# Performance work log

Measured on AMD Instinct MI355X. Metric: run time of the kernel, lower is better.

## Reference

```python
import jax, jax.numpy as jnp
import numpy as np

DIM, H, KVH = 1024, 16, 4
HD = DIM // H            # head_dim = 64
KV_DIM = KVH * HD        # 256
ROPE_BASE = 10000.0
EPS = 1e-6


def setup_inputs() -> dict:
    key = jax.random.key(0)
    ks = jax.random.split(key, 6)
    B, S = 4, 2048
    x = jax.random.normal(ks[0], (B, S, DIM), dtype=jnp.float32)
    sc = 0.02
    Wq = jax.random.normal(ks[1], (DIM, DIM), dtype=jnp.float32) * sc
    Wk = jax.random.normal(ks[2], (KV_DIM, DIM), dtype=jnp.float32) * sc
    Wv = jax.random.normal(ks[3], (KV_DIM, DIM), dtype=jnp.float32) * sc
    Wo = jax.random.normal(ks[4], (DIM, DIM), dtype=jnp.float32) * sc
    q_gain = jnp.full((H,), 1.5, dtype=jnp.float32)
    return {"x": x, "Wq": Wq, "Wk": Wk, "Wv": Wv, "Wo": Wo, "q_gain": q_gain}


def _rms_norm(t):
    return t * jax.lax.rsqrt(jnp.mean(t * t, axis=-1, keepdims=True) + EPS)


def _rotary(seqlen, dtype):
    inv_freq = 1.0 / (ROPE_BASE ** (jnp.arange(0, HD, 2, dtype=jnp.float32) / HD))
    t = jnp.arange(seqlen, dtype=jnp.float32)
    freqs = jnp.outer(t, inv_freq)                      # [S, HD/2]
    return jnp.cos(freqs).astype(dtype)[None, None], jnp.sin(freqs).astype(dtype)[None, None]


def _apply_rot(t, cos, sin):
    half = t.shape[-1] // 2
    t1, t2 = t[..., :half], t[..., half:]
    return jnp.concatenate((t1 * cos + t2 * sin, -t1 * sin + t2 * cos), axis=-1)


def reference(x, Wq, Wk, Wv, Wo, q_gain):
    B, S, D = x.shape
    q = (x @ Wq.T).reshape(B, S, H, HD).transpose(0, 2, 1, 3)      # [B,H,S,HD]
    k = (x @ Wk.T).reshape(B, S, KVH, HD).transpose(0, 2, 1, 3)    # [B,KVH,S,HD]
    v = (x @ Wv.T).reshape(B, S, KVH, HD).transpose(0, 2, 1, 3)
    q, k = _rms_norm(q), _rms_norm(k)
    cos, sin = _rotary(S, q.dtype)
    q, k = _apply_rot(q, cos, sin), _apply_rot(k, cos, sin)
    q = q * q_gain.astype(q.dtype)[None, :, None, None]
    rep = H // KVH
    k_exp = jnp.repeat(k, rep, axis=1)                              # GQA expand
    v_exp = jnp.repeat(v, rep, axis=1)
    scores = jnp.einsum('bhqd,bhkd->bhqk', q, k_exp) / np.sqrt(HD)
    causal = jnp.tril(jnp.ones((S, S), dtype=bool))
    scores = jnp.where(causal[None, None], scores, jnp.finfo(scores.dtype).min)
    attn = jax.nn.softmax(scores, axis=-1)
    y = jnp.einsum('bhqk,bhkd->bhqd', attn, v_exp)
    y = y.transpose(0, 2, 1, 3).reshape(B, S, D)
    return y @ Wo.T
```

## Files before the change

### kernel.cpp

```cpp
#include <hip/hip_runtime.h>

typedef float f32x4 __attribute__((ext_vector_type(4)));
typedef float f32x16 __attribute__((ext_vector_type(16)));
typedef __bf16 bf16x8 __attribute__((ext_vector_type(8)));
typedef unsigned short u16x8 __attribute__((ext_vector_type(8)));
typedef int i32x2 __attribute__((ext_vector_type(2)));
typedef int i32x4 __attribute__((ext_vector_type(4)));

#define DEV static __device__ __forceinline__

DEV float bf2f(unsigned short h) {
  unsigned int u = ((unsigned int)h) << 16;
  return __builtin_bit_cast(float, u);
}
DEV unsigned short f2bf(float f) {
  unsigned int u = __builtin_bit_cast(unsigned int, f);
  u += 0x7fff + ((u >> 16) & 1);
  return (unsigned short)(u >> 16);
}

DEV void g2l16(const void* g, void* l) {
  __builtin_amdgcn_global_load_lds(
      (const __attribute__((address_space(1))) void*)g,
      (__attribute__((address_space(3))) void*)l, 16, 0, 0);
}

DEV unsigned int cvtpk(float lo, float hi) {
  unsigned int r;
  asm("v_cvt_pk_bf16_f32 %0, %1, %2" : "=v"(r) : "v"(lo), "v"(hi));
  return r;
}

DEV float fexp2(float x) {
  float r;
  asm("v_exp_f32 %0, %1" : "=v"(r) : "v"(x));
  return r;
}

DEV void cvt8(const float* __restrict__ in, unsigned short* __restrict__ out, int idx) {
  int i = idx * 8;
  float4 a = *(const float4*)(in + i);
  float4 b = *(const float4*)(in + i + 4);
  u16x8 r;
  r[0] = f2bf(a.x); r[1] = f2bf(a.y); r[2] = f2bf(a.z); r[3] = f2bf(a.w);
  r[4] = f2bf(b.x); r[5] = f2bf(b.y); r[6] = f2bf(b.z); r[7] = f2bf(b.w);
  *(u16x8*)(out + i) = r;
}

__global__ __launch_bounds__(256) void k_cvt_all(const float* __restrict__ x,
                                                 const float* __restrict__ wq,
                                                 const float* __restrict__ wk,
                                                 const float* __restrict__ wv,
                                                 const float* __restrict__ wo,
                                                 unsigned short* __restrict__ xb,
                                                 unsigned short* __restrict__ wcat,
                                                 unsigned short* __restrict__ wob,
                                                 float2* __restrict__ rope) {
  const int blk = blockIdx.x, tid = threadIdx.x;
  if (blk < 4096) {
    cvt8(x, xb, blk * 256 + tid);
  } else if (blk < 4608) {
    cvt8(wq, wcat, (blk - 4096) * 256 + tid);
  } else if (blk < 4736) {
    cvt8(wk, wcat + 1048576, (blk - 4608) * 256 + tid);
  } else if (blk < 4864) {
    cvt8(wv, wcat + 1310720, (blk - 4736) * 256 + tid);
  } else if (blk < 5376) {
    cvt8(wo, wob, (blk - 4864) * 256 + tid);
  } else {
    int idx = (blk - 5376) * 256 + tid;
    int s = idx >> 5, dmod = idx & 31;
    float inv_freq = powf(10000.0f, -(float)dmod * (1.0f / 32.0f));
    float sn, cs;
    sincosf((float)s * inv_freq, &sn, &cs);
    rope[idx] = make_float2(cs, sn);
  }
}

__global__ __launch_bounds__(256) void k_qkv(const unsigned short* __restrict__ A,
                                             const unsigned short* __restrict__ B,
                                             const float* __restrict__ qg,
                                             const float2* __restrict__ rope,
                                             unsigned short* __restrict__ qn,
                                             unsigned short* __restrict__ kn2,
                                             unsigned short* __restrict__ vt2) {
  __shared__ unsigned short LDS[16384];
  unsigned short* As = LDS;
  unsigned short* Bs = LDS + 8192;
  const int K = 1024;
  const int tid = threadIdx.x;
  const int wid = tid >> 6, lane = tid & 63;
  const int g = lane >> 4, r16 = lane & 15;
  const int m0 = blockIdx.x * 128;
  const int y = blockIdx.y;
  const int n0 = y * 128;
  const int wr = wid >> 1, wc = wid & 1;

  f32x4 acc[4][4];
#pragma unroll
  for (int i = 0; i < 4; ++i)
#pragma unroll
    for (int j = 0; j < 4; ++j) acc[i][j] = f32x4{0.f, 0.f, 0.f, 0.f};

  const int cb = (lane & 7) * 16;

  for (int k0 = 0; k0 < K; k0 += 64) {
#pragma unroll
    for (int c = 0; c < 4; ++c) {
      int i = wid * 4 + c;
      int row = i * 8 + (lane >> 3);
      int sc = cb ^ ((row & 7) << 4);
      g2l16((const char*)A + ((size_t)(m0 + row) * K + k0) * 2 + sc, (char*)As + i * 1024);
      g2l16((const char*)B + ((size_t)(n0 + row) * K + k0) * 2 + sc, (char*)Bs + i * 1024);
    }
    __syncthreads();
#pragma unroll
    for (int kh = 0; kh < 2; ++kh) {
      bf16x8 af[4], bfr[4];
#pragma unroll
      for (int m = 0; m < 4; ++m) {
        int row = wr * 64 + m * 16 + r16;
        int byte = row * 128 + ((g * 16 + kh * 64) ^ ((row & 7) << 4));
        af[m] = *(const bf16x8*)((const char*)As + byte);
      }
#pragma unroll
      for (int n = 0; n < 4; ++n) {
        int row = wc * 64 + n * 16 + r16;
        int byte = row * 128 + ((g * 16 + kh * 64) ^ ((row & 7) << 4));
        bfr[n] = *(const bf16x8*)((const char*)Bs + byte);
      }
#pragma unroll
      for (int m = 0; m < 4; ++m)
#pragma unroll
        for (int n = 0; n < 4; ++n)
          acc[m][n] = __builtin_amdgcn_mfma_f32_16x16x32_bf16(af[m], bfr[n], acc[m][n], 0, 0, 0);
    }
    __syncthreads();
  }

  if (y < 10) {
    const bool isq = (y < 8);
    const int head = isq ? (2 * y + wc) : (2 * (y - 8) + wc);
    const float gain = isq ? qg[head] * 0.18033688011112042f : 1.0f;
    unsigned short* T = LDS;
#pragma unroll
    for (int m = 0; m < 4; ++m)
#pragma unroll
      for (int j = 0; j < 4; ++j) {
        int tokl = wr * 64 + m * 16 + g * 4 + j;
        int tok = m0 + tokl;
        int s = tok & 2047;
        float v0 = acc[m][0][j], v1 = acc[m][1][j], v2 = acc[m][2][j], v3 = acc[m][3][j];
        float ss = v0 * v0 + v1 * v1 + v2 * v2 + v3 * v3;
        ss += __shfl_xor(ss, 1); ss += __shfl_xor(ss, 2);
        ss += __shfl_xor(ss, 4); ss += __shfl_xor(ss, 8);
        float rs = rsqrtf(ss * (1.0f / 64.0f) + 1e-6f) * gain;
        float2 cs0 = rope[s * 32 + r16];
        float2 cs1 = rope[s * 32 + 16 + r16];
        float o0 = (v0 * cs0.x + v2 * cs0.y) * rs;
        float o2 = (v2 * cs0.x - v0 * cs0.y) * rs;
        float o1 = (v1 * cs1.x + v3 * cs1.y) * rs;
        float o3 = (v3 * cs1.x - v1 * cs1.y) * rs;
        char* rowb = (char*)T + tokl * 256;
        const int sw = (tokl & 15) << 4;
        const int dbase = wc * 128 + r16 * 2;
        *(unsigned short*)(rowb + ((dbase) ^ sw)) = f2bf(o0);
        *(unsigned short*)(rowb + ((dbase + 32) ^ sw)) = f2bf(o1);
        *(unsigned short*)(rowb + ((dbase + 64) ^ sw)) = f2bf(o2);
        *(unsigned short*)(rowb + ((dbase + 96) ^ sw)) = f2bf(o3);
      }
    __syncthreads();
    const int row0 = tid >> 4, cl = tid & 15;
    unsigned short* dstb = isq ? (qn + 2 * y * 64) : (kn2 + 2 * (y - 8) * 64);
    const int rstride = isq ? 1024 : 256;
#pragma unroll
    for (int it = 0; it < 8; ++it) {
      int row = it * 16 + row0;
      i32x4 w = *(const i32x4*)((const char*)T + row * 256 + ((cl * 16) ^ ((row & 15) << 4)));
      *(i32x4*)(dstb + (size_t)(m0 + row) * rstride + cl * 8) = w;
    }
  } else {
    unsigned short* T = LDS;
#pragma unroll
    for (int m = 0; m < 4; ++m)
#pragma unroll
      for (int n = 0; n < 4; ++n)
#pragma unroll
        for (int j = 0; j < 4; ++j) {
          int tokl = wr * 64 + m * 16 + g * 4 + j;
          int dl = wc * 64 + n * 16 + r16;
          int byte = (dl * 256 + tokl * 2) ^ ((dl & 15) << 4);
          *(unsigned short*)((char*)T + byte) = f2bf(acc[m][n][j]);
        }
    __syncthreads();
    const int d = tid >> 1, th = tid & 1;
    const int hv = 2 * (y - 10) + (d >> 6), dh = d & 63;
    const int bb = m0 >> 11;
    const int s0 = (m0 & 2047) + th * 64;
    const int kb64 = s0 >> 6;
    const int db = dh >> 5, d31 = dh & 31;
    const size_t vb0 = ((size_t)(bb * 4 + hv) * 32 + kb64) * 8 + db * 4;
    const int swz = (d & 15) << 4;
#pragma unroll
    for (int c = 0; c < 8; ++c) {
      i32x4 w = *(const i32x4*)((const char*)T + ((d * 256 + th * 128 + c * 16) ^ swz));
      *(i32x4*)(vt2 + (vb0 + (c >> 1)) * 512 + ((c & 1) * 32 + d31) * 8) = w;
    }
  }
}

__global__ __launch_bounds__(256) void k_krepack(const unsigned short* __restrict__ km,
                                                 unsigned short* __restrict__ kn2) {
  const int tid = threadIdx.x;
  const int bhv = blockIdx.y, kb = blockIdx.x;
  const int b = bhv >> 2, hv = bhv & 3;
  const int slot = tid & 63;
  const int m = tid >> 6;
  const int kw = slot & 31, hi8 = slot >> 5;
  const int key = kb * 32 + kw;
  const int d0 = m * 16 + hi8 * 8;
  u16x8 v = *(const u16x8*)(km + ((size_t)(b * 2048 + key)) * 256 + hv * 64 + d0);
  *(u16x8*)(kn2 + (((size_t)(bhv * 64 + kb) * 4 + m) * 512) + slot * 8) = v;
}

__global__ __launch_bounds__(256) void k_gemm_bt(const unsigned short* __restrict__ A,
                                                 const unsigned short* __restrict__ B,
                                                 float* __restrict__ C, int M, int N, int K) {
  __shared__ unsigned short As[128 * 64];
  __shared__ unsigned short Bs[128 * 64];
  const int tid = threadIdx.x;
  const int wid = tid >> 6, lane = tid & 63;
  const int g = lane >> 4, r16 = lane & 15;
  const int m0 = blockIdx.x * 128, n0 = blockIdx.y * 128;
  const int wr = wid >> 1, wc = wid & 1;

  f32x4 acc[4][4];
#pragma unroll
  for (int i = 0; i < 4; ++i)
#pragma unroll
    for (int j = 0; j < 4; ++j) acc[i][j] = f32x4{0.f, 0.f, 0.f, 0.f};

  const int cb = (lane & 7) * 16;

  for (int k0 = 0; k0 < K; k0 += 64) {
#pragma unroll
    for (int c = 0; c < 4; ++c) {
      int i = wid * 4 + c;
      int row = i * 8 + (lane >> 3);
      int sc = cb ^ ((row & 7) << 4);
      g2l16((const char*)A + ((size_t)(m0 + row) * K + k0) * 2 + sc, (char*)As + i * 1024);
      g2l16((const char*)B + ((size_t)(n0 + row) * K + k0) * 2 + sc, (char*)Bs + i * 1024);
    }
    __syncthreads();
#pragma unroll
    for (int kh = 0; kh < 2; ++kh) {
      bf16x8 af[4], bfr[4];
#pragma unroll
      for (int m = 0; m < 4; ++m) {
        int row = wr * 64 + m * 16 + r16;
        int byte = row * 128 + ((g * 16 + kh * 64) ^ ((row & 7) << 4));
        af[m] = *(const bf16x8*)((const char*)As + byte);
      }
#pragma unroll
      for (int n = 0; n < 4; ++n) {
        int row = wc * 64 + n * 16 + r16;
        int byte = row * 128 + ((g * 16 + kh * 64) ^ ((row & 7) << 4));
        bfr[n] = *(const bf16x8*)((const char*)Bs + byte);
      }
#pragma unroll
      for (int m = 0; m < 4; ++m)
#pragma unroll
        for (int n = 0; n < 4; ++n)
          acc[m][n] = __builtin_amdgcn_mfma_f32_16x16x32_bf16(af[m], bfr[n], acc[m][n], 0, 0, 0);
    }
    __syncthreads();
  }
#pragma unroll
  for (int m = 0; m < 4; ++m)
#pragma unroll
    for (int n = 0; n < 4; ++n)
#pragma unroll
      for (int j = 0; j < 4; ++j) {
        int row = m0 + wr * 64 + m * 16 + g * 4 + j;
        int col = n0 + wc * 64 + n * 16 + r16;
        C[(size_t)row * N + col] = acc[m][n][j];
      }
}

__global__ __launch_bounds__(512) void k_attn2(const unsigned short* __restrict__ qn,
                                               const unsigned short* __restrict__ kn2,
                                               const unsigned short* __restrict__ vt2,
                                               unsigned short* __restrict__ yb) {
  __shared__ unsigned short SMEM[4 * 8192];
  const int tid = threadIdx.x;
  const int wid = tid >> 6, lane = tid & 63;
  const int hi = lane >> 5, l31 = lane & 31;
  const int flat = blockIdx.x;
  const int qcx = 7 - (flat >> 6);
  const int bh = flat & 63;
  const int b = bh >> 4, h = bh & 15, hv = h >> 2;
  const int q0w = qcx * 256 + wid * 32;
  const int qglob = q0w + l31;
  const int tdiag = (q0w + 31) >> 6;
  const size_t tok0 = (size_t)b * 2048;

  const u16x8 onesu = {0x3F80, 0x3F80, 0x3F80, 0x3F80, 0x3F80, 0x3F80, 0x3F80, 0x3F80};
  const bf16x8 ones = __builtin_bit_cast(bf16x8, onesu);

  bf16x8 qf[4];
#pragma unroll
  for (int m = 0; m < 4; ++m)
    qf[m] = *(const bf16x8*)(qn + (tok0 + qglob) * 1024 + h * 64 + m * 16 + hi * 8);

  f32x16 oacc[2], lacc, zer;
#pragma unroll
  for (int r = 0; r < 16; ++r) { oacc[0][r] = 0.f; oacc[1][r] = 0.f; lacc[r] = 0.f; zer[r] = 0.f; }

  const int c0 = wid * 2;
  const unsigned short* src0;
  if (wid < 4) {
    src0 = kn2 + (size_t)(b * 4 + hv) * 131072 + c0 * 512 + lane * 8;
  } else {
    src0 = vt2 + (size_t)(b * 4 + hv) * 131072 + (c0 - 8) * 512 + lane * 8;
  }
  const unsigned short* src1 = src0 + 512;

  auto stage = [&](int T, int tb) {
    char* dst = (char*)SMEM + tb * 16384 + c0 * 1024;
    g2l16(src0 + (size_t)T * 4096, dst);
    g2l16(src1 + (size_t)T * 4096, dst + 1024);
  };

  const char* lbase = (const char*)SMEM + lane * 16;

  auto qk_tile = [&](int tb, f32x16* s) {
    const char* base = lbase + tb * 16384;
#pragma unroll
    for (int kt = 0; kt < 2; ++kt) {
      __builtin_amdgcn_s_setprio(1);
      bf16x8 kf = *(const bf16x8*)(base + (kt * 4) * 1024);
      f32x16 a = __builtin_amdgcn_mfma_f32_32x32x16_bf16(kf, qf[0], zer, 0, 0, 0);
#pragma unroll
      for (int m = 1; m < 4; ++m) {
        kf = *(const bf16x8*)(base + (kt * 4 + m) * 1024);
        a = __builtin_amdgcn_mfma_f32_32x32x16_bf16(kf, qf[m], a, 0, 0, 0);
      }
      __builtin_amdgcn_s_setprio(0);
      s[kt] = a;
    }
  };

  auto mask_tile = [&](int t, f32x16* s) {
    const int k0 = t * 64;
#pragma unroll
    for (int kt = 0; kt < 2; ++kt)
#pragma unroll
      for (int r = 0; r < 16; ++r) {
        int key = k0 + kt * 32 + (r & 3) + 8 * (r >> 2) + 4 * hi;
        if (key > qglob) s[kt][r] = -INFINITY;
      }
  };

  auto softmax_cvt = [&](f32x16* s, i32x4* paw) {
#pragma unroll
    for (int kt = 0; kt < 2; ++kt)
#pragma unroll
      for (int r = 0; r < 16; ++r) s[kt][r] = fexp2(s[kt][r]);
#pragma unroll
    for (int kt = 0; kt < 2; ++kt)
#pragma unroll
      for (int half = 0; half < 2; ++half) {
        int bs = half * 8;
        unsigned int a0 = cvtpk(s[kt][bs + 0], s[kt][bs + 1]);
        unsigned int a1 = cvtpk(s[kt][bs + 2], s[kt][bs + 3]);
        unsigned int b0 = cvtpk(s[kt][bs + 4], s[kt][bs + 5]);
        unsigned int b1 = cvtpk(s[kt][bs + 6], s[kt][bs + 7]);
        i32x2 r0 = __builtin_amdgcn_permlane32_swap((int)a0, (int)b0, false, false);
        i32x2 r1 = __builtin_amdgcn_permlane32_swap((int)a1, (int)b1, false, false);
        i32x4 w;
        w[0] = r0[0]; w[1] = r1[0]; w[2] = r0[1]; w[3] = r1[1];
        paw[kt * 2 + half] = w;
      }
  };

  auto pv_tile = [&](int tb, const i32x4* paw) {
    const char* base = lbase + tb * 16384 + 8192;
    __builtin_amdgcn_s_setprio(1);
#pragma unroll
    for (int db = 0; db < 2; ++db)
#pragma unroll
      for (int ks = 0; ks < 4; ++ks) {
        bf16x8 vf = *(const bf16x8*)(base + (db * 4 + ks) * 1024);
        oacc[db] = __builtin_amdgcn_mfma_f32_32x32x16_bf16(
            vf, __builtin_bit_cast(bf16x8, paw[ks]), oacc[db], 0, 0, 0);
      }
#pragma unroll
    for (int ks = 0; ks < 4; ++ks)
      lacc = __builtin_amdgcn_mfma_f32_32x32x16_bf16(
          ones, __builtin_bit_cast(bf16x8, paw[ks]), lacc, 0, 0, 0);
    __builtin_amdgcn_s_setprio(0);
  };

  const int npair = 2 * qcx + 2;

  stage(0, 0);
  stage(1, 1);
  __syncthreads();

  for (int p = 0; p < npair; ++p) {
    const int pb = (p & 1) << 1;
    if (p + 1 < npair) {
      stage(2 * p + 2, pb ^ 2);
      stage(2 * p + 3, (pb ^ 2) | 1);
    }
    const int t0 = 2 * p;
    const bool visa = (t0 <= tdiag), visb = (t0 + 1 <= tdiag);
    const bool domask = (p >= npair - 2);
    f32x16 sa[2], sb[2];
    if (visa) qk_tile(pb, sa);
    if (visb) qk_tile(pb | 1, sb);
    if (domask) {
      if (visa) mask_tile(t0, sa);
      if (visb) mask_tile(t0 + 1, sb);
    }
    i32x4 pawa[4], pawb[4];
    if (visa) {
      softmax_cvt(sa, pawa);
      pv_tile(pb, pawa);
    }
    if (visb) {
      softmax_cvt(sb, pawb);
      pv_tile(pb | 1, pawb);
    }
    __syncthreads();
  }

  const float inv = 1.0f / lacc[0];
  const int swl = (l31 & 7) << 4;
  char* obase = (char*)SMEM + wid * 4096;
#pragma unroll
  for (int db = 0; db < 2; ++db)
#pragma unroll
    for (int i = 0; i < 8; ++i) {
      int r = 2 * i;
      int dim = db * 32 + (r & 3) + 8 * (r >> 2) + 4 * hi;
      unsigned int w = (unsigned int)f2bf(oacc[db][r] * inv) |
                       ((unsigned int)f2bf(oacc[db][r + 1] * inv) << 16);
      *(unsigned int*)(obase + l31 * 128 + ((dim * 2) ^ swl)) = w;
    }
  __syncthreads();
#pragma unroll
  for (int it = 0; it < 4; ++it) {
    int cc = it * 2 + hi;
    i32x4 w = *(const i32x4*)(obase + l31 * 128 + ((cc * 16) ^ swl));
    *(i32x4*)(yb + (tok0 + q0w + l31) * 1024 + h * 64 + cc * 8) = w;
  }
}

extern "C" void kernel_launch(void* const* d_in, const int* in_sizes, int n_in,
                              void* d_out, int out_size, void* d_ws, size_t ws_size,
                              hipStream_t stream) {
  (void)in_sizes; (void)n_in; (void)out_size; (void)ws_size;
  const float* x  = (const float*)d_in[0];
  const float* Wq = (const float*)d_in[1];
  const float* Wk = (const float*)d_in[2];
  const float* Wv = (const float*)d_in[3];
  const float* Wo = (const float*)d_in[4];
  const float* qg = (const float*)d_in[5];

  char* ws = (char*)d_ws;
  unsigned short* xb   = (unsigned short*)(ws);
  unsigned short* wcat = (unsigned short*)(ws + 16777216);
  unsigned short* wob  = (unsigned short*)(ws + 19922944);
  unsigned short* qn   = (unsigned short*)(ws + 22020096);
  unsigned short* km   = (unsigned short*)(ws + 38797312);
  unsigned short* kn2  = (unsigned short*)(ws + 43253760);
  unsigned short* yb   = xb;
  unsigned short* vt2  = (unsigned short*)((char*)d_out + 25165824);
  float2*         rope = (float2*)((char*)d_out + 29360128);

  k_cvt_all<<<5632, 256, 0, stream>>>(x, Wq, Wk, Wv, Wo, xb, wcat, wob, rope);
  k_qkv<<<dim3(64, 12), 256, 0, stream>>>(xb, wcat, qg, rope, qn, km, vt2);
  k_krepack<<<dim3(64, 16), 256, 0, stream>>>(km, kn2);
  k_attn2<<<512, 512, 0, stream>>>(qn, kn2, vt2, yb);
  k_gemm_bt<<<dim3(64, 8), 256, 0, stream>>>(yb, wob, (float*)d_out, 8192, 1024, 1024);
}
```

Before: 136.1 us.

## Fuse K repack into QKV epilogue and give attention warps two query blocks

The QKV projection epilogue now writes K directly into the blocked layout the attention kernel consumes, which removes the separate repack kernel and its round trip through global memory. The attention kernel drops from 8 to 4 warps per block. Each warp now handles 64 queries as two 32-row blocks that share each K/V fragment read from LDS, and each warp stages four chunks per tile. The row-sum MFMA against a ones vector is replaced by a scalar sum plus a cross-half shuffle, which trades matrix-unit work for VALU adds but increases register pressure and lowers the number of waves per block.

```diff
diff --git a/kernel.cpp b/kernel.cpp
--- a/kernel.cpp
+++ b/kernel.cpp
@@ -170,14 +170,32 @@
         *(unsigned short*)(rowb + ((dbase + 96) ^ sw)) = f2bf(o3);
       }
     __syncthreads();
-    const int row0 = tid >> 4, cl = tid & 15;
-    unsigned short* dstb = isq ? (qn + 2 * y * 64) : (kn2 + 2 * (y - 8) * 64);
-    const int rstride = isq ? 1024 : 256;
-#pragma unroll
-    for (int it = 0; it < 8; ++it) {
-      int row = it * 16 + row0;
-      i32x4 w = *(const i32x4*)((const char*)T + row * 256 + ((cl * 16) ^ ((row & 15) << 4)));
-      *(i32x4*)(dstb + (size_t)(m0 + row) * rstride + cl * 8) = w;
+    if (isq) {
+      const int row0 = tid >> 4, cl = tid & 15;
+      unsigned short* dstb = qn + 2 * y * 64;
+#pragma unroll
+      for (int it = 0; it < 8; ++it) {
+        int row = it * 16 + row0;
+        i32x4 w = *(const i32x4*)((const char*)T + row * 256 + ((cl * 16) ^ ((row & 15) << 4)));
+        *(i32x4*)(dstb + (size_t)(m0 + row) * 1024 + cl * 8) = w;
+      }
+    } else {
+      const int b_ = m0 >> 11;
+      const int kb0 = (m0 & 2047) >> 5;
+      const int fu = tid >> 3, sub = tid & 7;
+      const int hsel = fu >> 4, kb = (fu >> 2) & 3, m = fu & 3;
+      const int headk = 2 * (y - 8) + hsel;
+      unsigned short* dst =
+          kn2 + ((size_t)((b_ * 4 + headk) * 64 + kb0 + kb) * 4 + m) * 512;
+#pragma unroll
+      for (int k = 0; k < 8; ++k) {
+        int slot = k * 8 + sub;
+        int kw = slot & 31, hi8 = slot >> 5;
+        int tokl = kb * 32 + kw;
+        int d0 = hsel * 64 + m * 16 + hi8 * 8;
+        i32x4 w = *(const i32x4*)((const char*)T + tokl * 256 + ((d0 * 2) ^ ((tokl & 15) << 4)));
+        *(i32x4*)(dst + slot * 8) = w;
+      }
     }
   } else {
     unsigned short* T = LDS;
@@ -207,20 +225,6 @@
       *(i32x4*)(vt2 + (vb0 + (c >> 1)) * 512 + ((c & 1) * 32 + d31) * 8) = w;
     }
   }
-}
-
-__global__ __launch_bounds__(256) void k_krepack(const unsigned short* __restrict__ km,
-                                                 unsigned short* __restrict__ kn2) {
-  const int tid = threadIdx.x;
-  const int bhv = blockIdx.y, kb = blockIdx.x;
-  const int b = bhv >> 2, hv = bhv & 3;
-  const int slot = tid & 63;
-  const int m = tid >> 6;
-  const int kw = slot & 31, hi8 = slot >> 5;
-  const int key = kb * 32 + kw;
-  const int d0 = m * 16 + hi8 * 8;
-  u16x8 v = *(const u16x8*)(km + ((size_t)(b * 2048 + key)) * 256 + hv * 64 + d0);
-  *(u16x8*)(kn2 + (((size_t)(bhv * 64 + kb) * 4 + m) * 512) + slot * 8) = v;
 }
 
 __global__ __launch_bounds__(256) void k_gemm_bt(const unsigned short* __restrict__ A,
@@ -287,7 +291,7 @@
       }
 }
 
-__global__ __launch_bounds__(512) void k_attn2(const unsigned short* __restrict__ qn,
+__global__ __launch_bounds__(256) void k_attn2(const unsigned short* __restrict__ qn,
                                                const unsigned short* __restrict__ kn2,
                                                const unsigned short* __restrict__ vt2,
                                                unsigned short* __restrict__ yb) {
@@ -299,73 +303,50 @@
   const int qcx = 7 - (flat >> 6);
   const int bh = flat & 63;
   const int b = bh >> 4, h = bh & 15, hv = h >> 2;
-  const int q0w = qcx * 256 + wid * 32;
-  const int qglob = q0w + l31;
-  const int tdiag = (q0w + 31) >> 6;
+  const int q0w = qcx * 256 + wid * 64;
+  const int qglob0 = q0w + l31, qglob1 = q0w + 32 + l31;
+  const int tdiag0 = (q0w + 31) >> 6, tdiag1 = (q0w + 63) >> 6;
   const size_t tok0 = (size_t)b * 2048;
 
-  const u16x8 onesu = {0x3F80, 0x3F80, 0x3F80, 0x3F80, 0x3F80, 0x3F80, 0x3F80, 0x3F80};
-  const bf16x8 ones = __builtin_bit_cast(bf16x8, onesu);
-
-  bf16x8 qf[4];
-#pragma unroll
-  for (int m = 0; m < 4; ++m)
-    qf[m] = *(const bf16x8*)(qn + (tok0 + qglob) * 1024 + h * 64 + m * 16 + hi * 8);
-
-  f32x16 oacc[2], lacc, zer;
-#pragma unroll
-  for (int r = 0; r < 16; ++r) { oacc[0][r] = 0.f; oacc[1][r] = 0.f; lacc[r] = 0.f; zer[r] = 0.f; }
-
-  const int c0 = wid * 2;
-  const unsigned short* src0;
-  if (wid < 4) {
-    src0 = kn2 + (size_t)(b * 4 + hv) * 131072 + c0 * 512 + lane * 8;
-  } else {
-    src0 = vt2 + (size_t)(b * 4 + hv) * 131072 + (c0 - 8) * 512 + lane * 8;
-  }
-  const unsigned short* src1 = src0 + 512;
+  bf16x8 qf0[4], qf1[4];
+#pragma unroll
+  for (int m = 0; m < 4; ++m) {
+    qf0[m] = *(const bf16x8*)(qn + (tok0 + qglob0) * 1024 + h * 64 + m * 16 + hi * 8);
+    qf1[m] = *(const bf16x8*)(qn + (tok0 + qglob1) * 1024 + h * 64 + m * 16 + hi * 8);
+  }
+
+  f32x16 oacc[2][2], zer;
+#pragma unroll
+  for (int r = 0; r < 16; ++r) {
+    oacc[0][0][r] = 0.f; oacc[0][1][r] = 0.f;
+    oacc[1][0][r] = 0.f; oacc[1][1][r] = 0.f;
+    zer[r] = 0.f;
+  }
+  float lsum[2] = {0.f, 0.f};
+
+  const unsigned short* srcb =
+      ((wid < 2) ? kn2 : vt2) + (size_t)(b * 4 + hv) * 131072 + ((wid & 1) * 4) * 512 + lane * 8;
 
   auto stage = [&](int T, int tb) {
-    char* dst = (char*)SMEM + tb * 16384 + c0 * 1024;
-    g2l16(src0 + (size_t)T * 4096, dst);
-    g2l16(src1 + (size_t)T * 4096, dst + 1024);
+    char* dst = (char*)SMEM + tb * 16384 + wid * 4096;
+    const unsigned short* s = srcb + (size_t)T * 4096;
+#pragma unroll
+    for (int f = 0; f < 4; ++f) g2l16(s + f * 512, dst + f * 1024);
   };
 
   const char* lbase = (const char*)SMEM + lane * 16;
 
-  auto qk_tile = [&](int tb, f32x16* s) {
-    const char* base = lbase + tb * 16384;
-#pragma unroll
-    for (int kt = 0; kt < 2; ++kt) {
-      __builtin_amdgcn_s_setprio(1);
-      bf16x8 kf = *(const bf16x8*)(base + (kt * 4) * 1024);
-      f32x16 a = __builtin_amdgcn_mfma_f32_32x32x16_bf16(kf, qf[0], zer, 0, 0, 0);
-#pragma unroll
-      for (int m = 1; m < 4; ++m) {
-        kf = *(const bf16x8*)(base + (kt * 4 + m) * 1024);
-        a = __builtin_amdgcn_mfma_f32_32x32x16_bf16(kf, qf[m], a, 0, 0, 0);
-      }
-      __builtin_amdgcn_s_setprio(0);
-      s[kt] = a;
-    }
-  };
-
-  auto mask_tile = [&](int t, f32x16* s) {
-    const int k0 = t * 64;
+  auto softmax_cvt = [&](f32x16* s, i32x4* paw, int qb) {
 #pragma unroll
     for (int kt = 0; kt < 2; ++kt)
 #pragma unroll
-      for (int r = 0; r < 16; ++r) {
-        int key = k0 + kt * 32 + (r & 3) + 8 * (r >> 2) + 4 * hi;
-        if (key > qglob) s[kt][r] = -INFINITY;
-      }
-  };
-
-  auto softmax_cvt = [&](f32x16* s, i32x4* paw) {
+      for (int r = 0; r < 16; ++r) s[kt][r] = fexp2(s[kt][r]);
+    float t0 = 0.f;
 #pragma unroll
     for (int kt = 0; kt < 2; ++kt)
 #pragma unroll
-      for (int r = 0; r < 16; ++r) s[kt][r] = fexp2(s[kt][r]);
+      for (int r = 0; r < 16; ++r) t0 += s[kt][r];
+    lsum[qb] += t0;
 #pragma unroll
     for (int kt = 0; kt < 2; ++kt)
 #pragma unroll
@@ -383,21 +364,52 @@
       }
   };
 
-  auto pv_tile = [&](int tb, const i32x4* paw) {
-    const char* base = lbase + tb * 16384 + 8192;
+  auto tile = [&](int t, int tb, bool domask) {
+    if (t > tdiag1) return;
+    const bool vis0 = (t <= tdiag0);
+    const char* kbase = lbase + tb * 16384;
+    f32x16 s0[2], s1[2];
     __builtin_amdgcn_s_setprio(1);
 #pragma unroll
+    for (int kt = 0; kt < 2; ++kt) {
+      bf16x8 kf = *(const bf16x8*)(kbase + (kt * 4) * 1024);
+      s1[kt] = __builtin_amdgcn_mfma_f32_32x32x16_bf16(kf, qf1[0], zer, 0, 0, 0);
+      if (vis0) s0[kt] = __builtin_amdgcn_mfma_f32_32x32x16_bf16(kf, qf0[0], zer, 0, 0, 0);
+#pragma unroll
+      for (int m = 1; m < 4; ++m) {
+        kf = *(const bf16x8*)(kbase + (kt * 4 + m) * 1024);
+        s1[kt] = __builtin_amdgcn_mfma_f32_32x32x16_bf16(kf, qf1[m], s1[kt], 0, 0, 0);
+        if (vis0) s0[kt] = __builtin_amdgcn_mfma_f32_32x32x16_bf16(kf, qf0[m], s0[kt], 0, 0, 0);
+      }
+    }
+    __builtin_amdgcn_s_setprio(0);
+    if (domask) {
+      const int k0 = t * 64;
+#pragma unroll
+      for (int kt = 0; kt < 2; ++kt)
+#pragma unroll
+        for (int r = 0; r < 16; ++r) {
+          int key = k0 + kt * 32 + (r & 3) + 8 * (r >> 2) + 4 * hi;
+          if (key > qglob1) s1[kt][r] = -INFINITY;
+          if (vis0 && key > qglob0) s0[kt][r] = -INFINITY;
+        }
+    }
+    i32x4 paw0[4], paw1[4];
+    if (vis0) softmax_cvt(s0, paw0, 0);
+    softmax_cvt(s1, paw1, 1);
+    const char* vbase = lbase + tb * 16384 + 8192;
+    __builtin_amdgcn_s_setprio(1);
+#pragma unroll
     for (int db = 0; db < 2; ++db)
 #pragma unroll
       for (int ks = 0; ks < 4; ++ks) {
-        bf16x8 vf = *(const bf16x8*)(base + (db * 4 + ks) * 1024);
-        oacc[db] = __builtin_amdgcn_mfma_f32_32x32x16_bf16(
-            vf, __builtin_bit_cast(bf16x8, paw[ks]), oacc[db], 0, 0, 0);
-      }
-#pragma unroll
-    for (int ks = 0; ks < 4; ++ks)
-      lacc = __builtin_amdgcn_mfma_f32_32x32x16_bf16(
-          ones, __builtin_bit_cast(bf16x8, paw[ks]), lacc, 0, 0, 0);
+        bf16x8 vf = *(const bf16x8*)(vbase + (db * 4 + ks) * 1024);
+        oacc[1][db] = __builtin_amdgcn_mfma_f32_32x32x16_bf16(
+            vf, __builtin_bit_cast(bf16x8, paw1[ks]), oacc[1][db], 0, 0, 0);
+        if (vis0)
+          oacc[0][db] = __builtin_amdgcn_mfma_f32_32x32x16_bf16(
+              vf, __builtin_bit_cast(bf16x8, paw0[ks]), oacc[0][db], 0, 0, 0);
+      }
     __builtin_amdgcn_s_setprio(0);
   };
 
@@ -413,47 +425,37 @@
       stage(2 * p + 2, pb ^ 2);
       stage(2 * p + 3, (pb ^ 2) | 1);
     }
-    const int t0 = 2 * p;
-    const bool visa = (t0 <= tdiag), visb = (t0 + 1 <= tdiag);
     const bool domask = (p >= npair - 2);
-    f32x16 sa[2], sb[2];
-    if (visa) qk_tile(pb, sa);
-    if (visb) qk_tile(pb | 1, sb);
-    if (domask) {
-      if (visa) mask_tile(t0, sa);
-      if (visb) mask_tile(t0 + 1, sb);
-    }
-    i32x4 pawa[4], pawb[4];
-    if (visa) {
-      softmax_cvt(sa, pawa);
-      pv_tile(pb, pawa);
-    }
-    if (visb) {
-      softmax_cvt(sb, pawb);
-      pv_tile(pb | 1, pawb);
-    }
-    __syncthreads();
-  }
-
-  const float inv = 1.0f / lacc[0];
+    tile(2 * p, pb, domask);
+    tile(2 * p + 1, pb | 1, domask);
+    __syncthreads();
+  }
+
+  lsum[0] += __shfl_xor(lsum[0], 32);
+  lsum[1] += __shfl_xor(lsum[1], 32);
   const int swl = (l31 & 7) << 4;
   char* obase = (char*)SMEM + wid * 4096;
 #pragma unroll
-  for (int db = 0; db < 2; ++db)
-#pragma unroll
-    for (int i = 0; i < 8; ++i) {
-      int r = 2 * i;
-      int dim = db * 32 + (r & 3) + 8 * (r >> 2) + 4 * hi;
-      unsigned int w = (unsigned int)f2bf(oacc[db][r] * inv) |
-                       ((unsigned int)f2bf(oacc[db][r + 1] * inv) << 16);
-      *(unsigned int*)(obase + l31 * 128 + ((dim * 2) ^ swl)) = w;
-    }
-  __syncthreads();
-#pragma unroll
-  for (int it = 0; it < 4; ++it) {
-    int cc = it * 2 + hi;
-    i32x4 w = *(const i32x4*)(obase + l31 * 128 + ((cc * 16) ^ swl));
-    *(i32x4*)(yb + (tok0 + q0w + l31) * 1024 + h * 64 + cc * 8) = w;
+  for (int qb = 0; qb < 2; ++qb) {
+    const float inv = 1.0f / lsum[qb];
+#pragma unroll
+    for (int db = 0; db < 2; ++db)
+#pragma unroll
+      for (int i = 0; i < 8; ++i) {
+        int r = 2 * i;
+        int dim = db * 32 + (r & 3) + 8 * (r >> 2) + 4 * hi;
+        unsigned int w = (unsigned int)f2bf(oacc[qb][db][r] * inv) |
+                         ((unsigned int)f2bf(oacc[qb][db][r + 1] * inv) << 16);
+        *(unsigned int*)(obase + l31 * 128 + ((dim * 2) ^ swl)) = w;
+      }
+    __syncthreads();
+#pragma unroll
+    for (int it = 0; it < 4; ++it) {
+      int cc = it * 2 + hi;
+      i32x4 w = *(const i32x4*)(obase + l31 * 128 + ((cc * 16) ^ swl));
+      *(i32x4*)(yb + (tok0 + q0w + qb * 32 + l31) * 1024 + h * 64 + cc * 8) = w;
+    }
+    __syncthreads();
   }
 }
 
@@ -473,15 +475,13 @@
   unsigned short* wcat = (unsigned short*)(ws + 16777216);
   unsigned short* wob  = (unsigned short*)(ws + 19922944);
   unsigned short* qn   = (unsigned short*)(ws + 22020096);
-  unsigned short* km   = (unsigned short*)(ws + 38797312);
-  unsigned short* kn2  = (unsigned short*)(ws + 43253760);
+  unsigned short* kn2  = (unsigned short*)(ws + 38797312);
   unsigned short* yb   = xb;
   unsigned short* vt2  = (unsigned short*)((char*)d_out + 25165824);
   float2*         rope = (float2*)((char*)d_out + 29360128);
 
   k_cvt_all<<<5632, 256, 0, stream>>>(x, Wq, Wk, Wv, Wo, xb, wcat, wob, rope);
-  k_qkv<<<dim3(64, 12), 256, 0, stream>>>(xb, wcat, qg, rope, qn, km, vt2);
-  k_krepack<<<dim3(64, 16), 256, 0, stream>>>(km, kn2);
-  k_attn2<<<512, 512, 0, stream>>>(qn, kn2, vt2, yb);
+  k_qkv<<<dim3(64, 12), 256, 0, stream>>>(xb, wcat, qg, rope, qn, kn2, vt2);
+  k_attn2<<<512, 256, 0, stream>>>(qn, kn2, vt2, yb);
   k_gemm_bt<<<dim3(64, 8), 256, 0, stream>>>(yb, wob, (float*)d_out, 8192, 1024, 1024);
 }
```

Result: slower. 143.7 us (+5.6%).
